# Kernel tuning notes

Hardware: AMD Instinct MI355X
Metric: run time of the kernel (lower is better)

Reference implementation:

```python
import jax, jax.numpy as jnp
import numpy as np
import math

B, T, L, C = 4, 8, 512, 768
H = 8
HD = C // H  # 96
EPS = 1e-12  # F.normalize eps


def _l2norm(x):
    # F.normalize(x, dim=-1): x / max(||x||2, eps)
    n = jnp.sqrt(jnp.sum(x * x, axis=-1, keepdims=True))
    return x / jnp.maximum(n, EPS)


def setup_inputs() -> dict:
    key = jax.random.key(0)
    ks = jax.random.split(key, 7)
    s = 1.0 / math.sqrt(C)
    x = jax.random.normal(ks[0], (B, T, L, C), dtype=jnp.float32)
    Wq = jax.random.uniform(ks[1], (C, C), jnp.float32, -s, s)
    bq = jax.random.uniform(ks[2], (C,), jnp.float32, -s, s)
    Wkv = jax.random.uniform(ks[3], (C, 2 * C), jnp.float32, -s, s)
    bkv = jax.random.uniform(ks[4], (2 * C,), jnp.float32, -s, s)
    Wm = jax.random.uniform(ks[5], (C, C), jnp.float32, -s, s)
    bm = jax.random.uniform(ks[6], (C,), jnp.float32, -s, s)
    return {"x": x, "Wq": Wq, "bq": bq, "Wkv": Wkv, "bkv": bkv, "Wm": Wm, "bm": bm}


def reference(x, Wq, bq, Wkv, bkv, Wm, bm):
    b, t, l, c = x.shape
    # q: (b,t,l,c) -> (b,t,H,l,hd), L2-normalized over hd
    q = (x @ Wq + bq).reshape(b, t, l, H, HD).transpose(0, 1, 3, 2, 4)
    q = _l2norm(q)
    # kv: (b,t,l,2c) -> (b,t,2H,l,hd); chunk on head axis -> k = heads [0,H), v = heads [H,2H)
    kv = (x @ Wkv + bkv).reshape(b, t, l, 2 * H, HD).transpose(0, 1, 3, 2, 4)
    k = _l2norm(kv[:, :, :H])
    v = _l2norm(kv[:, :, H:])
    # attention (dropout on scores is identity in eval mode)
    scores = jnp.einsum("bthqd,bthkd->bthqk", q, k) / math.sqrt(HD)
    attn = jax.nn.softmax(scores, axis=-1)
    out = jnp.einsum("bthqk,bthkd->bthqd", attn, v)
    # (b,t,H,l,hd) -> (b,t,l,c), output projection (drop2 identity in eval)
    out = out.transpose(0, 1, 3, 2, 4).reshape(b, t, l, c)
    return out @ Wm + bm
```

## Files before the change

kernel.cpp:

```cpp
#include <hip/hip_runtime.h>
#include <hip/hip_bf16.h>


typedef __attribute__((ext_vector_type(8))) short bf16x8;
typedef __attribute__((ext_vector_type(4))) float f32x4;
typedef __attribute__((ext_vector_type(4))) int int4v;

__device__ __forceinline__ float b2f(unsigned short u) {
    return __uint_as_float(((unsigned)u) << 16);
}
__device__ __forceinline__ unsigned short f2b(float f) {
    unsigned u = __float_as_uint(f);
    u = (u + 0x7fffu + ((u >> 16) & 1u)) >> 16;
    return (unsigned short)u;
}

__device__ __forceinline__ void gll16(const unsigned short* g, unsigned short* l) {
    __builtin_amdgcn_global_load_lds((const __attribute__((address_space(1))) unsigned int*)g,
                                     (__attribute__((address_space(3))) unsigned int*)l, 16, 0, 0);
}

#define VMCNT(n) asm volatile("s_waitcnt vmcnt(" #n ")" ::: "memory")
#define BAR()    __builtin_amdgcn_s_barrier()
#define SCHED0() __builtin_amdgcn_sched_barrier(0)
#define PRIO(x)  __builtin_amdgcn_s_setprio(x)

__global__ __launch_bounds__(256) void prep_k(const float* __restrict__ x,
                                              unsigned short* __restrict__ xb,
                                              const float* __restrict__ Wq,
                                              const float* __restrict__ Wkv,
                                              const float* __restrict__ Wm,
                                              unsigned short* __restrict__ Wt) {
    __shared__ float tile[64][65];
    const int tid = threadIdx.x;
    if (blockIdx.x < 12288) {
        const int i = blockIdx.x * 256 + tid;
        float4 v = ((const float4*)x)[i];
        ushort4 o;
        o.x = f2b(v.x); o.y = f2b(v.y); o.z = f2b(v.z); o.w = f2b(v.w);
        ((ushort4*)xb)[i] = o;
        return;
    }
    const int pb = blockIdx.x - 12288;
    const int tn = pb % 48;
    const int tk = pb / 48;
    const int n0 = tn * 64, k0 = tk * 64;
    const float* src; int ldn, coff;
    if (n0 < 768)       { src = Wq;  ldn = 768;  coff = n0; }
    else if (n0 < 2304) { src = Wkv; ldn = 1536; coff = n0 - 768; }
    else                { src = Wm;  ldn = 768;  coff = n0 - 2304; }
    const int j = tid & 63;
    for (int i = tid >> 6; i < 64; i += 4)
        tile[i][j] = src[(k0 + i) * ldn + coff + j];
    __syncthreads();
    const int ii = tid & 63;
    for (int jj = tid >> 6; jj < 64; jj += 4)
        Wt[(long)(n0 + jj) * 768 + k0 + ii] = f2b(tile[ii][jj]);
}

template <int EPI>
__global__ __launch_bounds__(512, 4) void gemm_k(const unsigned short* __restrict__ A,
                                                 const unsigned short* __restrict__ Bt,
                                                 const float* __restrict__ bias0,
                                                 const float* __restrict__ bias1,
                                                 unsigned short* __restrict__ Cb,
                                                 float* __restrict__ Cf,
                                                 int N, int K, int nbn) {
    extern __shared__ unsigned short lds[];
    const int tid = threadIdx.x;
    const int lane = tid & 63, wid = tid >> 6;
    const int wm = wid >> 1, wn = wid & 1;
    const int l15 = lane & 15, g = lane >> 4;

    const int nwg = gridDim.x;
    const int wg = (blockIdx.x & 7) * (nwg >> 3) + (blockIdx.x >> 3);
    const int bm = wg / nbn, bn = wg % nbn;

    const unsigned short* gA = A  + (long)bm * 256 * K;
    const unsigned short* gB = Bt + (long)bn * 128 * K;

    const long sgoff = (long)(tid >> 2) * K + (long)(((tid & 3) ^ ((tid >> 3) & 3)) * 8);
    const int swoff = wid * 512;

#define STAGE_ALL(T, BUFO) do { \
        const long kb0 = (long)(T) * 32; \
        gll16(gB + sgoff + kb0, lds + (BUFO) + 8192 + swoff); \
        gll16(gA + sgoff + kb0, lds + (BUFO) + swoff); \
        gll16(gA + sgoff + kb0 + (long)128 * K, lds + (BUFO) + 4096 + swoff); \
    } while (0)

    const int slot8 = (g ^ ((l15 >> 1) & 3)) * 8;
    f32x4 acc[4][4] = {};
    const int nkt = K >> 5;

    STAGE_ALL(0, 0);
    STAGE_ALL(1, 12288);

    int cur = 0, nx1 = 12288, nx2 = 24576;
    for (int t = 0; t < nkt; ++t) {
        if (t < nkt - 1) { VMCNT(3); } else { VMCNT(0); }
        BAR(); SCHED0();
        if (t + 2 < nkt) STAGE_ALL(t + 2, nx2);

        bf16x8 af[4], bv[4];
#pragma unroll
        for (int mf = 0; mf < 4; mf++)
            af[mf] = *(const bf16x8*)&lds[cur + (wm * 64 + mf * 16 + l15) * 32 + slot8];
#pragma unroll
        for (int nf = 0; nf < 4; nf++)
            bv[nf] = *(const bf16x8*)&lds[cur + 8192 + (wn * 64 + nf * 16 + l15) * 32 + slot8];
        PRIO(1);
#pragma unroll
        for (int mf = 0; mf < 4; mf++)
#pragma unroll
            for (int nf = 0; nf < 4; nf++)
                acc[mf][nf] = __builtin_amdgcn_mfma_f32_16x16x32_bf16(af[mf], bv[nf], acc[mf][nf], 0, 0, 0);
        PRIO(0);
        const int tmp = cur; cur = nx1; nx1 = nx2; nx2 = tmp;
    }
#undef STAGE_ALL

    float bvv[4];
#pragma unroll
    for (int nf = 0; nf < 4; nf++) {
        const int col = bn * 128 + wn * 64 + nf * 16 + l15;
        bvv[nf] = (EPI == 0) ? ((col < 768) ? bias0[col] : bias1[col - 768]) : bias0[col];
    }
#pragma unroll
    for (int mf = 0; mf < 4; mf++) {
#pragma unroll
        for (int r = 0; r < 4; r++) {
            const long row = bm * 256 + wm * 64 + mf * 16 + g * 4 + r;
#pragma unroll
            for (int nf = 0; nf < 4; nf++) {
                const float v = acc[mf][nf][r] + bvv[nf];
                if (EPI == 0) {
                    const unsigned hh = f2b(v);
                    const unsigned oo = __shfl_xor((int)hh, 1);
                    if (!(lane & 1))
                        *(unsigned*)&Cb[row * N + bn * 128 + wn * 64 + nf * 16 + l15] =
                            (hh & 0xffffu) | (oo << 16);
                } else {
                    Cf[row * N + bn * 128 + wn * 64 + nf * 16 + l15] = v;
                }
            }
        }
    }
}

__global__ __launch_bounds__(512, 6) void gemm128_k(const unsigned short* __restrict__ A,
                                                    const unsigned short* __restrict__ Bt,
                                                    const float* __restrict__ bias0,
                                                    float* __restrict__ Cf,
                                                    int N, int K, int nbn) {
    extern __shared__ unsigned short lds[];
    const int tid = threadIdx.x;
    const int lane = tid & 63, wid = tid >> 6;
    const int wm = wid >> 2, wn = wid & 3;
    const int l15 = lane & 15, g = lane >> 4;

    const int nwg = gridDim.x;
    const int wg = (blockIdx.x & 7) * (nwg >> 3) + (blockIdx.x >> 3);
    const int bm = wg / nbn, bn = wg % nbn;

    const unsigned short* gA = A  + (long)bm * 128 * K;
    const unsigned short* gB = Bt + (long)bn * 128 * K;

    const long sgoff = (long)(tid >> 2) * K + (long)(((tid & 3) ^ ((tid >> 3) & 3)) * 8);
    const int swoff = wid * 512;

#define STAGE2(T, BUFO) do { \
        const long kb0 = (long)(T) * 32; \
        gll16(gB + sgoff + kb0, lds + (BUFO) + 4096 + swoff); \
        gll16(gA + sgoff + kb0, lds + (BUFO) + swoff); \
    } while (0)

    const int slot8 = (g ^ ((l15 >> 1) & 3)) * 8;
    f32x4 acc[4][2] = {};
    const int nkt = K >> 5;

    STAGE2(0, 0);
    STAGE2(1, 8192);

    int cur = 0, nx1 = 8192, nx2 = 16384;
    for (int t = 0; t < nkt; ++t) {
        if (t < nkt - 1) { VMCNT(2); } else { VMCNT(0); }
        BAR(); SCHED0();
        if (t + 2 < nkt) STAGE2(t + 2, nx2);

        bf16x8 af[4], bv[2];
#pragma unroll
        for (int mf = 0; mf < 4; mf++)
            af[mf] = *(const bf16x8*)&lds[cur + (wm * 64 + mf * 16 + l15) * 32 + slot8];
#pragma unroll
        for (int nf = 0; nf < 2; nf++)
            bv[nf] = *(const bf16x8*)&lds[cur + 4096 + (wn * 32 + nf * 16 + l15) * 32 + slot8];
        PRIO(1);
#pragma unroll
        for (int mf = 0; mf < 4; mf++)
#pragma unroll
            for (int nf = 0; nf < 2; nf++)
                acc[mf][nf] = __builtin_amdgcn_mfma_f32_16x16x32_bf16(af[mf], bv[nf], acc[mf][nf], 0, 0, 0);
        PRIO(0);
        const int tmp = cur; cur = nx1; nx1 = nx2; nx2 = tmp;
    }
#undef STAGE2

    float bvv[2];
#pragma unroll
    for (int nf = 0; nf < 2; nf++)
        bvv[nf] = bias0[bn * 128 + wn * 32 + nf * 16 + l15];
#pragma unroll
    for (int mf = 0; mf < 4; mf++) {
#pragma unroll
        for (int r = 0; r < 4; r++) {
            const long row = bm * 128 + wm * 64 + mf * 16 + g * 4 + r;
#pragma unroll
            for (int nf = 0; nf < 2; nf++)
                Cf[row * N + bn * 128 + wn * 32 + nf * 16 + l15] = acc[mf][nf][r] + bvv[nf];
        }
    }
}

__global__ __launch_bounds__(256) void knvn_k(const unsigned short* __restrict__ qkv,
                                              float* __restrict__ kinv,
                                              float* __restrict__ vinv) {
    const int tid = threadIdx.x, lane = tid & 63, w = tid >> 6;
    const int s = blockIdx.x * 4 + w;
    const int row = s >> 3, h = s & 7;
    const unsigned short* pk = qkv + (long)row * 2304 + 768 + h * 96;
    float k0 = 0.f, k1 = 0.f, v0 = 0.f, v1 = 0.f;
    if (lane < 48) {
        unsigned a = *(const unsigned*)(pk + lane * 2);
        unsigned b = *(const unsigned*)(pk + 768 + lane * 2);
        k0 = b2f((unsigned short)(a & 0xffffu)); k1 = b2f((unsigned short)(a >> 16));
        v0 = b2f((unsigned short)(b & 0xffffu)); v1 = b2f((unsigned short)(b >> 16));
    }
    float sk = k0 * k0 + k1 * k1;
    float sv = v0 * v0 + v1 * v1;
#pragma unroll
    for (int m = 1; m < 64; m <<= 1) { sk += __shfl_xor(sk, m); sv += __shfl_xor(sv, m); }
    if (lane == 0) {
        kinv[h * 16384 + row] = 1.f / fmaxf(sqrtf(sk), 1e-12f);
        vinv[h * 16384 + row] = 1.f / fmaxf(sqrtf(sv), 1e-12f);
    }
}

__global__ __launch_bounds__(512, 2) void attn_k(const unsigned short* __restrict__ qkv,
                                                 const float* __restrict__ kinv,
                                                 const float* __restrict__ vinv,
                                                 unsigned short* __restrict__ obuf) {
    constexpr float SCALE = 0.1020620726159658f;
    __shared__ unsigned short Ps[128 * 72];
    __shared__ unsigned short Ks[2][64 * 104];
    __shared__ unsigned short Vt[2][96 * 72];
    __shared__ float kinv_s[2][64], vinv_s[2][64];

    const int tid = threadIdx.x, lane = tid & 63, w = tid >> 6;
    const int bid0 = blockIdx.x;
    const int bid = (bid0 & 7) * 128 + (bid0 >> 3);
    const int qt = bid & 3, h = (bid >> 2) & 7, bt = bid >> 5;
    const long rowbase = (long)bt * 512 * 2304 + h * 96;
    const int l15 = lane & 15;
    const int g = lane >> 4;
    const int ko = g * 8;

    bf16x8 qf[3];
    {
        const unsigned short* qrow = qkv + rowbase + (long)(qt * 128 + w * 16 + l15) * 2304;
#pragma unroll
        for (int ks = 0; ks < 3; ks++)
            qf[ks] = *(const bf16x8*)&qrow[ks * 32 + ko];
    }

    if (tid < 256) {
#pragma unroll
        for (int j = 0; j < 3; j++) {
            const int c = tid + j * 256;
            const int r = c / 12, d8 = (c % 12) * 8;
            *(int4v*)&Ks[0][r * 104 + d8] = *(const int4v*)&qkv[rowbase + 768 + (long)r * 2304 + d8];
        }
    } else {
        const int tid2 = tid - 256;
#pragma unroll
        for (int j = 0; j < 2; j++) {
            const int c = tid2 + j * 256;
            if (c < 384) {
                const int kp = c & 31, d8c = c >> 5;
                const unsigned short* vsrc = &qkv[rowbase + 1536 + (long)(2 * kp) * 2304 + d8c * 8];
                int4v v0 = *(const int4v*)vsrc;
                int4v v1 = *(const int4v*)(vsrc + 2304);
                const unsigned short* p0 = (const unsigned short*)&v0;
                const unsigned short* p1 = (const unsigned short*)&v1;
#pragma unroll
                for (int i = 0; i < 8; i++)
                    *(unsigned*)&Vt[0][(d8c * 8 + i) * 72 + 2 * kp] =
                        (unsigned)p0[i] | ((unsigned)p1[i] << 16);
            }
        }
    }
    if (tid < 64)       kinv_s[0][tid]      = kinv[h * 16384 + bt * 512 + tid];
    else if (tid < 128) vinv_s[0][tid - 64] = vinv[h * 16384 + bt * 512 + tid - 64];
    __syncthreads();

    float ssq = 0.f;
#pragma unroll
    for (int ks = 0; ks < 3; ks++)
#pragma unroll
        for (int j = 0; j < 8; j++) {
            const float f = b2f((unsigned short)qf[ks][j]);
            ssq += f * f;
        }
    ssq += __shfl_xor(ssq, 16);
    ssq += __shfl_xor(ssq, 32);
    const float qs = SCALE / fmaxf(sqrtf(ssq), 1e-12f);

    float l_run = 0.f;
    f32x4 oacc[6] = {};

    for (int kt = 0; kt < 8; kt++) {
        const int cb = kt & 1, nb = cb ^ 1;

        int4v preg[4];
        float tn = 0.f;
        if (kt < 7) {
            if (tid < 256) {
                const long kb = rowbase + 768 + (long)((kt + 1) * 64) * 2304;
#pragma unroll
                for (int j = 0; j < 3; j++) {
                    const int c = tid + j * 256;
                    preg[j] = *(const int4v*)&qkv[kb + (long)(c / 12) * 2304 + (c % 12) * 8];
                }
            } else {
                const int tid2 = tid - 256;
                const long vb = rowbase + 1536 + (long)((kt + 1) * 64) * 2304;
#pragma unroll
                for (int j = 0; j < 2; j++) {
                    const int c = tid2 + j * 256;
                    if (c < 384) {
                        const int kp = c & 31, d8c = c >> 5;
                        const unsigned short* vsrc = &qkv[vb + (long)(2 * kp) * 2304 + d8c * 8];
                        preg[2 * j]     = *(const int4v*)vsrc;
                        preg[2 * j + 1] = *(const int4v*)(vsrc + 2304);
                    }
                }
            }
            if (tid < 64)       tn = kinv[h * 16384 + bt * 512 + (kt + 1) * 64 + tid];
            else if (tid < 128) tn = vinv[h * 16384 + bt * 512 + (kt + 1) * 64 + tid - 64];
        }

        f32x4 sacc[4] = {};
        PRIO(1);
#pragma unroll
        for (int ks = 0; ks < 3; ks++) {
#pragma unroll
            for (int kf = 0; kf < 4; kf++) {
                bf16x8 af = *(const bf16x8*)&Ks[cb][(kf * 16 + l15) * 104 + ks * 32 + ko];
                sacc[kf] = __builtin_amdgcn_mfma_f32_16x16x32_bf16(af, qf[ks], sacc[kf], 0, 0, 0);
            }
        }
        PRIO(0);

        float p[16];
        float s = 0.f;
#pragma unroll
        for (int kf = 0; kf < 4; kf++)
#pragma unroll
            for (int r = 0; r < 4; r++) {
                const float pv = __expf(sacc[kf][r] * qs * kinv_s[cb][kf * 16 + g * 4 + r]);
                s += pv;
                p[kf * 4 + r] = pv * vinv_s[cb][kf * 16 + g * 4 + r];
            }
        s += __shfl_xor(s, 16);
        s += __shfl_xor(s, 32);
        l_run += s;

        {
            unsigned* prow = (unsigned*)&Ps[(w * 16 + l15) * 72];
#pragma unroll
            for (int kf = 0; kf < 4; kf++)
#pragma unroll
                for (int rp = 0; rp < 2; rp++) {
                    unsigned pk = (unsigned)f2b(p[kf * 4 + 2 * rp]) |
                                  ((unsigned)f2b(p[kf * 4 + 2 * rp + 1]) << 16);
                    prow[kf * 8 + g * 2 + rp] = pk;
                }
        }

        PRIO(1);
#pragma unroll
        for (int ks = 0; ks < 2; ks++) {
            bf16x8 pa = *(const bf16x8*)&Ps[(w * 16 + l15) * 72 + ks * 32 + ko];
#pragma unroll
            for (int nf = 0; nf < 6; nf++) {
                bf16x8 vb = *(const bf16x8*)&Vt[cb][(nf * 16 + l15) * 72 + ks * 32 + ko];
                oacc[nf] = __builtin_amdgcn_mfma_f32_16x16x32_bf16(pa, vb, oacc[nf], 0, 0, 0);
            }
        }
        PRIO(0);

        if (kt < 7) {
            if (tid < 256) {
#pragma unroll
                for (int j = 0; j < 3; j++) {
                    const int c = tid + j * 256;
                    *(int4v*)&Ks[nb][(c / 12) * 104 + (c % 12) * 8] = preg[j];
                }
            } else {
                const int tid2 = tid - 256;
#pragma unroll
                for (int j = 0; j < 2; j++) {
                    const int c = tid2 + j * 256;
                    if (c < 384) {
                        const int kp = c & 31, d8c = c >> 5;
                        const unsigned short* p0 = (const unsigned short*)&preg[2 * j];
                        const unsigned short* p1 = (const unsigned short*)&preg[2 * j + 1];
#pragma unroll
                        for (int i = 0; i < 8; i++)
                            *(unsigned*)&Vt[nb][(d8c * 8 + i) * 72 + 2 * kp] =
                                (unsigned)p0[i] | ((unsigned)p1[i] << 16);
                    }
                }
            }
            if (tid < 64)       kinv_s[nb][tid]      = tn;
            else if (tid < 128) vinv_s[nb][tid - 64] = tn;
            __syncthreads();
        }
    }

    const float inv = 1.f / l_run;
    float invr[4];
#pragma unroll
    for (int r = 0; r < 4; r++) invr[r] = __shfl(inv, g * 4 + r);
#pragma unroll
    for (int r = 0; r < 4; r++) {
        const int row = w * 16 + g * 4 + r;
        const long gr = ((long)(bt * 512 + qt * 128 + row)) * 768 + h * 96;
#pragma unroll
        for (int nf = 0; nf < 6; nf++)
            obuf[gr + nf * 16 + l15] = f2b(oacc[nf][r] * invr[r]);
    }
}

extern "C" void kernel_launch(void* const* d_in, const int* in_sizes, int n_in,
                              void* d_out, int out_size, void* d_ws, size_t ws_size,
                              hipStream_t stream) {
    const float* x   = (const float*)d_in[0];
    const float* Wq  = (const float*)d_in[1];
    const float* bq  = (const float*)d_in[2];
    const float* Wkv = (const float*)d_in[3];
    const float* bkv = (const float*)d_in[4];
    const float* Wm  = (const float*)d_in[5];
    const float* bm  = (const float*)d_in[6];
    float* out = (float*)d_out;

    char* ws = (char*)d_ws;
    unsigned short* xb  = (unsigned short*)ws;
    float*          vinv = (float*)ws;
    float*          kinv = (float*)(ws + 524288);
    unsigned short* wt  = (unsigned short*)(ws + 25165824);
    unsigned short* qkv = (unsigned short*)(ws + 29884416);
    unsigned short* ob  = (unsigned short*)(ws + 105381888);

    static bool attr_set = false;
    if (!attr_set) {
        hipFuncSetAttribute((const void*)gemm_k<0>, hipFuncAttributeMaxDynamicSharedMemorySize, 73728);
        hipFuncSetAttribute((const void*)gemm128_k, hipFuncAttributeMaxDynamicSharedMemorySize, 49152);
        attr_set = true;
    }

    prep_k<<<dim3(12864), dim3(256), 0, stream>>>(x, xb, Wq, Wkv, Wm, wt);
    gemm_k<0><<<dim3(1152), dim3(512), 73728, stream>>>(xb, wt, bq, bkv, qkv, nullptr, 2304, 768, 18);
    knvn_k<<<dim3(32768), dim3(256), 0, stream>>>(qkv, kinv, vinv);
    attn_k<<<dim3(1024), dim3(512), 0, stream>>>(qkv, kinv, vinv, ob);
    gemm128_k<<<dim3(768), dim3(512), 49152, stream>>>(ob, wt + (long)2304 * 768, bm, out, 768, 768, 6);
}
```

Baseline: 192.6 us.

## Fuse K/V L2-norm computation into attention kernel, dropping separate norm pass

Removes the standalone knvn_k kernel that re-read K and V from global memory to compute per-row inverse norms. The attention kernel now computes partial sums of squares from the K/V tiles it already loads, stores them in shared memory, reduces them to per-row inverse norms, and uses them in place of the precomputed global arrays. This saves one kernel launch and a full extra read of K/V, at the cost of some extra ALU work per tile and an additional block-wide barrier in every key-tile iteration.

```diff
diff --git a/kernel.cpp b/kernel.cpp
--- a/kernel.cpp
+++ b/kernel.cpp
@@ -222,39 +222,15 @@
     }
 }
 
-__global__ __launch_bounds__(256) void knvn_k(const unsigned short* __restrict__ qkv,
-                                              float* __restrict__ kinv,
-                                              float* __restrict__ vinv) {
-    const int tid = threadIdx.x, lane = tid & 63, w = tid >> 6;
-    const int s = blockIdx.x * 4 + w;
-    const int row = s >> 3, h = s & 7;
-    const unsigned short* pk = qkv + (long)row * 2304 + 768 + h * 96;
-    float k0 = 0.f, k1 = 0.f, v0 = 0.f, v1 = 0.f;
-    if (lane < 48) {
-        unsigned a = *(const unsigned*)(pk + lane * 2);
-        unsigned b = *(const unsigned*)(pk + 768 + lane * 2);
-        k0 = b2f((unsigned short)(a & 0xffffu)); k1 = b2f((unsigned short)(a >> 16));
-        v0 = b2f((unsigned short)(b & 0xffffu)); v1 = b2f((unsigned short)(b >> 16));
-    }
-    float sk = k0 * k0 + k1 * k1;
-    float sv = v0 * v0 + v1 * v1;
-#pragma unroll
-    for (int m = 1; m < 64; m <<= 1) { sk += __shfl_xor(sk, m); sv += __shfl_xor(sv, m); }
-    if (lane == 0) {
-        kinv[h * 16384 + row] = 1.f / fmaxf(sqrtf(sk), 1e-12f);
-        vinv[h * 16384 + row] = 1.f / fmaxf(sqrtf(sv), 1e-12f);
-    }
-}
-
 __global__ __launch_bounds__(512, 2) void attn_k(const unsigned short* __restrict__ qkv,
-                                                 const float* __restrict__ kinv,
-                                                 const float* __restrict__ vinv,
                                                  unsigned short* __restrict__ obuf) {
     constexpr float SCALE = 0.1020620726159658f;
     __shared__ unsigned short Ps[128 * 72];
     __shared__ unsigned short Ks[2][64 * 104];
     __shared__ unsigned short Vt[2][96 * 72];
-    __shared__ float kinv_s[2][64], vinv_s[2][64];
+    __shared__ float ksum_p[768];
+    __shared__ float vsum_p[768];
+    __shared__ float kinv_s[64], vinv_s[64];
 
     const int tid = threadIdx.x, lane = tid & 63, w = tid >> 6;
     const int bid0 = blockIdx.x;
@@ -278,7 +254,13 @@
         for (int j = 0; j < 3; j++) {
             const int c = tid + j * 256;
             const int r = c / 12, d8 = (c % 12) * 8;
-            *(int4v*)&Ks[0][r * 104 + d8] = *(const int4v*)&qkv[rowbase + 768 + (long)r * 2304 + d8];
+            int4v kv = *(const int4v*)&qkv[rowbase + 768 + (long)r * 2304 + d8];
+            *(int4v*)&Ks[0][r * 104 + d8] = kv;
+            const unsigned short* kp8 = (const unsigned short*)&kv;
+            float s8 = 0.f;
+#pragma unroll
+            for (int i = 0; i < 8; i++) { const float f = b2f(kp8[i]); s8 += f * f; }
+            ksum_p[c] = s8;
         }
     } else {
         const int tid2 = tid - 256;
@@ -292,15 +274,19 @@
                 int4v v1 = *(const int4v*)(vsrc + 2304);
                 const unsigned short* p0 = (const unsigned short*)&v0;
                 const unsigned short* p1 = (const unsigned short*)&v1;
-#pragma unroll
-                for (int i = 0; i < 8; i++)
+                float s0 = 0.f, s1 = 0.f;
+#pragma unroll
+                for (int i = 0; i < 8; i++) {
+                    const float f0 = b2f(p0[i]); s0 += f0 * f0;
+                    const float f1 = b2f(p1[i]); s1 += f1 * f1;
                     *(unsigned*)&Vt[0][(d8c * 8 + i) * 72 + 2 * kp] =
                         (unsigned)p0[i] | ((unsigned)p1[i] << 16);
-            }
-        }
-    }
-    if (tid < 64)       kinv_s[0][tid]      = kinv[h * 16384 + bt * 512 + tid];
-    else if (tid < 128) vinv_s[0][tid - 64] = vinv[h * 16384 + bt * 512 + tid - 64];
+                }
+                vsum_p[d8c * 64 + 2 * kp]     = s0;
+                vsum_p[d8c * 64 + 2 * kp + 1] = s1;
+            }
+        }
+    }
     __syncthreads();
 
     float ssq = 0.f;
@@ -322,7 +308,6 @@
         const int cb = kt & 1, nb = cb ^ 1;
 
         int4v preg[4];
-        float tn = 0.f;
         if (kt < 7) {
             if (tid < 256) {
                 const long kb = rowbase + 768 + (long)((kt + 1) * 64) * 2304;
@@ -345,8 +330,18 @@
                     }
                 }
             }
-            if (tid < 64)       tn = kinv[h * 16384 + bt * 512 + (kt + 1) * 64 + tid];
-            else if (tid < 128) tn = vinv[h * 16384 + bt * 512 + (kt + 1) * 64 + tid - 64];
+        }
+
+        if (tid < 64) {
+            float s = 0.f;
+#pragma unroll
+            for (int m = 0; m < 12; m++) s += ksum_p[tid * 12 + m];
+            kinv_s[tid] = 1.f / fmaxf(sqrtf(s), 1e-12f);
+        } else if (tid < 128) {
+            float s = 0.f;
+#pragma unroll
+            for (int m = 0; m < 12; m++) s += vsum_p[m * 64 + (tid - 64)];
+            vinv_s[tid - 64] = 1.f / fmaxf(sqrtf(s), 1e-12f);
         }
 
         f32x4 sacc[4] = {};
@@ -361,15 +356,17 @@
         }
         PRIO(0);
 
+        __syncthreads();
+
         float p[16];
         float s = 0.f;
 #pragma unroll
         for (int kf = 0; kf < 4; kf++)
 #pragma unroll
             for (int r = 0; r < 4; r++) {
-                const float pv = __expf(sacc[kf][r] * qs * kinv_s[cb][kf * 16 + g * 4 + r]);
+                const float pv = __expf(sacc[kf][r] * qs * kinv_s[kf * 16 + g * 4 + r]);
                 s += pv;
-                p[kf * 4 + r] = pv * vinv_s[cb][kf * 16 + g * 4 + r];
+                p[kf * 4 + r] = pv * vinv_s[kf * 16 + g * 4 + r];
             }
         s += __shfl_xor(s, 16);
         s += __shfl_xor(s, 32);
@@ -405,6 +402,11 @@
                 for (int j = 0; j < 3; j++) {
                     const int c = tid + j * 256;
                     *(int4v*)&Ks[nb][(c / 12) * 104 + (c % 12) * 8] = preg[j];
+                    const unsigned short* kp8 = (const unsigned short*)&preg[j];
+                    float s8 = 0.f;
+#pragma unroll
+                    for (int i = 0; i < 8; i++) { const float f = b2f(kp8[i]); s8 += f * f; }
+                    ksum_p[c] = s8;
                 }
             } else {
                 const int tid2 = tid - 256;
@@ -415,15 +417,19 @@
                         const int kp = c & 31, d8c = c >> 5;
                         const unsigned short* p0 = (const unsigned short*)&preg[2 * j];
                         const unsigned short* p1 = (const unsigned short*)&preg[2 * j + 1];
-#pragma unroll
-                        for (int i = 0; i < 8; i++)
+                        float s0 = 0.f, s1 = 0.f;
+#pragma unroll
+                        for (int i = 0; i < 8; i++) {
+                            const float f0 = b2f(p0[i]); s0 += f0 * f0;
+                            const float f1 = b2f(p1[i]); s1 += f1 * f1;
                             *(unsigned*)&Vt[nb][(d8c * 8 + i) * 72 + 2 * kp] =
                                 (unsigned)p0[i] | ((unsigned)p1[i] << 16);
+                        }
+                        vsum_p[d8c * 64 + 2 * kp]     = s0;
+                        vsum_p[d8c * 64 + 2 * kp + 1] = s1;
                     }
                 }
             }
-            if (tid < 64)       kinv_s[nb][tid]      = tn;
-            else if (tid < 128) vinv_s[nb][tid - 64] = tn;
             __syncthreads();
         }
     }
@@ -456,8 +462,6 @@
 
     char* ws = (char*)d_ws;
     unsigned short* xb  = (unsigned short*)ws;
-    float*          vinv = (float*)ws;
-    float*          kinv = (float*)(ws + 524288);
     unsigned short* wt  = (unsigned short*)(ws + 25165824);
     unsigned short* qkv = (unsigned short*)(ws + 29884416);
     unsigned short* ob  = (unsigned short*)(ws + 105381888);
@@ -471,7 +475,6 @@
 
     prep_k<<<dim3(12864), dim3(256), 0, stream>>>(x, xb, Wq, Wkv, Wm, wt);
     gemm_k<0><<<dim3(1152), dim3(512), 73728, stream>>>(xb, wt, bq, bkv, qkv, nullptr, 2304, 768, 18);
-    knvn_k<<<dim3(32768), dim3(256), 0, stream>>>(qkv, kinv, vinv);
-    attn_k<<<dim3(1024), dim3(512), 0, stream>>>(qkv, kinv, vinv, ob);
+    attn_k<<<dim3(1024), dim3(512), 0, stream>>>(qkv, ob);
     gemm128_k<<<dim3(768), dim3(512), 49152, stream>>>(ob, wt + (long)2304 * 768, bm, out, 768, 768, 6);
 }
```

New measurement: 174.3 us. -9.5%, faster.
